# Kernel tuning notes

Measured on AMD Instinct MI355X. Metric: run time of the kernel, lower is better.

## Reference

```python
import jax, jax.numpy as jnp
import numpy as np

B, S, H, K = 64, 512, 768, 21  # batch, seq_len, bert hidden, num_labels


def setup_inputs() -> dict:
    key = jax.random.key(0)
    ks = jax.random.split(key, 8)
    hidden = jax.random.normal(ks[0], (B, S, H), jnp.float32)  # post-BERT states
    W = jax.random.normal(ks[1], (H, K), jnp.float32) * 0.02    # classifier weight
    b = jnp.zeros((K,), jnp.float32)                            # classifier bias
    start_transitions = jax.random.uniform(ks[2], (K,), jnp.float32, -0.1, 0.1)
    transitions = jax.random.uniform(ks[3], (K, K), jnp.float32, -0.1, 0.1)
    end_transitions = jax.random.uniform(ks[4], (K,), jnp.float32, -0.1, 0.1)
    labels = jax.random.randint(ks[5], (B, S), 0, K)
    # torchcrf requires mask[:, 0] == 1; use variable-length prefix masks
    lengths = jax.random.randint(ks[6], (B,), S // 2, S + 1)
    attention_mask = jnp.arange(S)[None, :] < lengths[:, None]  # [B,S] bool
    return dict(hidden=hidden, W=W, b=b,
                start_transitions=start_transitions,
                transitions=transitions,
                end_transitions=end_transitions,
                labels=labels, attention_mask=attention_mask)


def _crf_nll(logits, labels, mask, start_t, trans, end_t):
    """torchcrf CRF forward (reduction='sum' log-likelihood), negated."""
    fmask = mask.astype(logits.dtype)  # [B,S]
    # ---- numerator: score of the gold path ----
    emit = jnp.take_along_axis(logits, labels[..., None], axis=2)[..., 0]  # [B,S]
    tr = trans[labels[:, :-1], labels[:, 1:]]                              # [B,S-1]
    num = start_t[labels[:, 0]] + emit[:, 0] \
        + jnp.sum((emit[:, 1:] + tr) * fmask[:, 1:], axis=1)
    lengths = mask.sum(axis=1)
    last_tags = jnp.take_along_axis(labels, (lengths - 1)[:, None], axis=1)[:, 0]
    num = num + end_t[last_tags]
    # ---- denominator: forward algorithm (logsumexp recurrence) ----
    alpha0 = start_t[None, :] + logits[:, 0]           # [B,K]
    ems = jnp.swapaxes(logits[:, 1:], 0, 1)            # [S-1,B,K]
    ms = jnp.swapaxes(mask[:, 1:], 0, 1)               # [S-1,B]

    def step(alpha, xs):
        em, m = xs
        nxt = jax.scipy.special.logsumexp(
            alpha[:, :, None] + trans[None, :, :] + em[:, None, :], axis=1)
        return jnp.where(m[:, None], nxt, alpha), None

    alpha, _ = jax.lax.scan(step, alpha0, (ems, ms))
    logZ = jax.scipy.special.logsumexp(alpha + end_t[None, :], axis=1)  # [B]
    return jnp.sum(logZ - num)  # negative log-likelihood (sum over batch)


def reference(hidden, W, b, start_transitions, transitions, end_transitions,
              labels, attention_mask):
    # dropout is identity in eval; the GRU in __init__ is unused in forward
    logits = hidden @ W + b  # [B,S,K]
    nll = _crf_nll(logits, labels, attention_mask,
                   start_transitions, transitions, end_transitions)
    # module returns (logits, -1 * log_likelihood) = (logits, nll)
    return (logits, nll)
```

## Files before the change

### kernel.cpp

```cpp
#include <hip/hip_runtime.h>

#define BSZ 64
#define SEQ 512
#define HID 768
#define NK  21
#define NSEG 32
#define SEGLEN 16
#define PSTR 512

typedef short bf16x8 __attribute__((ext_vector_type(8)));
typedef float f32x4  __attribute__((ext_vector_type(4)));

__device__ __forceinline__ unsigned f2bf1(float x) {
    unsigned u = __float_as_uint(x);
    return (u + 0x7fffu + ((u >> 16) & 1u)) >> 16;
}
__device__ __forceinline__ unsigned f2bf_pk(float lo, float hi) {
    return f2bf1(lo) | (f2bf1(hi) << 16);
}

#define U16L(d) __uint_as_float(((unsigned)(d)) << 16)
#define U16H(d) __uint_as_float(((unsigned)(d)) & 0xffff0000u)

__global__ __launch_bounds__(256) void wconv_len_kernel(
    const float* __restrict__ W, const int* __restrict__ mask,
    unsigned short* __restrict__ WT, int* __restrict__ Lbuf,
    float* __restrict__ out)
{
    if (blockIdx.x < 96) {
        const int idx = blockIdx.x * 256 + threadIdx.x;
        const int n = idx / HID;
        const int k = idx - n * HID;
        unsigned short v = 0;
        if (n < NK) v = (unsigned short)f2bf1(W[(size_t)k * NK + n]);
        WT[idx] = v;
    } else {
        const int tid = threadIdx.x;
        if (tid == 255) out[BSZ * SEQ * NK] = 0.f;
        const int b = tid >> 2, q = tid & 3;
        const int* msk = mask + b * SEQ + q * 128;
        int cnt = 0;
        for (int r = 0; r < 128; ++r) cnt += (msk[r] != 0);
        cnt += __shfl_xor(cnt, 1, 64);
        cnt += __shfl_xor(cnt, 2, 64);
        if (q == 0 && b < BSZ) Lbuf[b] = cnt;
    }
}

__global__ __launch_bounds__(256) void gemm_bias_kernel(
    const float* __restrict__ hidden, const unsigned short* __restrict__ WT,
    const float* __restrict__ bias, float* __restrict__ out)
{
    const int tid  = threadIdx.x;
    const int lane = tid & 63;
    const int wv   = tid >> 6;
    const int n    = lane & 15;
    const int quad = lane >> 4;

    const int arow = blockIdx.x * 64 + wv * 16 + n;
    const float* ap = hidden + (size_t)arow * HID + quad * 8;
    const bf16x8* bp0 = (const bf16x8*)(WT + (size_t)n * HID + quad * 8);
    const bf16x8* bp1 = (const bf16x8*)(WT + (size_t)(16 + n) * HID + quad * 8);

    f32x4 acc0 = {0.f, 0.f, 0.f, 0.f};
    f32x4 acc1 = {0.f, 0.f, 0.f, 0.f};

    float4 a0 = *(const float4*)(ap + 0);
    float4 a1 = *(const float4*)(ap + 4);
    float4 p0 = *(const float4*)(ap + 32);
    float4 p1 = *(const float4*)(ap + 36);
    bf16x8 B0 = bp0[0];
    bf16x8 B1 = bp1[0];

    #pragma unroll
    for (int c = 0; c < HID / 32; ++c) {
        float4 q0, q1; bf16x8 Bn0, Bn1;
        if (c + 2 < HID / 32) {
            q0 = *(const float4*)(ap + (c + 2) * 32);
            q1 = *(const float4*)(ap + (c + 2) * 32 + 4);
        }
        if (c + 1 < HID / 32) {
            Bn0 = bp0[(c + 1) * 4];
            Bn1 = bp1[(c + 1) * 4];
        }
        union { bf16x8 v; unsigned u[4]; } af;
        af.u[0] = f2bf_pk(a0.x, a0.y);
        af.u[1] = f2bf_pk(a0.z, a0.w);
        af.u[2] = f2bf_pk(a1.x, a1.y);
        af.u[3] = f2bf_pk(a1.z, a1.w);

        acc0 = __builtin_amdgcn_mfma_f32_16x16x32_bf16(af.v, B0, acc0, 0, 0, 0);
        acc1 = __builtin_amdgcn_mfma_f32_16x16x32_bf16(af.v, B1, acc1, 0, 0, 0);

        a0 = p0; a1 = p1; p0 = q0; p1 = q1;
        B0 = Bn0; B1 = Bn1;
    }

    const float b0v = bias[n];
    const float b1v = (n < NK - 16) ? bias[16 + n] : 0.f;
    const int rbase = blockIdx.x * 64 + wv * 16 + quad * 4;
    #pragma unroll
    for (int r = 0; r < 4; ++r) {
        float* op = out + (size_t)(rbase + r) * NK;
        op[n] = acc0[r] + b0v;
        if (n < NK - 16) op[16 + n] = acc1[r] + b1v;
    }
}

#define EHI(u) __uint_as_float((u) & 0xffff0000u)
#define ELO(u) __uint_as_float((u) << 16)
__global__ __launch_bounds__(64, 2) void prepass_kernel(
    const float* __restrict__ logits, const float* __restrict__ trans,
    const int* __restrict__ Lbuf,
    unsigned short* __restrict__ Nrowb, unsigned short* __restrict__ Ncolb,
    float* __restrict__ rlog)
{
    const int bs   = blockIdx.x;
    const int b    = bs >> 5;
    const int s    = bs & 31;
    const int lane = threadIdx.x;
    int g = lane / 21; if (g > 2) g = 2;
    int i = lane - g * 21; if (i > 20) i = 20;
    const int j0 = 7 * g;

    const int L = Lbuf[b];

    unsigned Epk[7][11];
    #pragma unroll
    for (int jl = 0; jl < 7; ++jl)
        #pragma unroll
        for (int p = 0; p < 11; ++p) {
            const float ehi = __expf(trans[(2 * p) * NK + j0 + jl]);
            const float elo = (2 * p + 1 < 21)
                            ? __expf(trans[(2 * p + 1) * NK + j0 + jl]) : 0.f;
            Epk[jl][p] = (f2bf1(ehi) << 16) | f2bf1(elo);
        }

    const float* lg = logits + (size_t)b * SEQ * NK;

    float P[7];
    float rl = 0.f;
    const int t0 = s * SEGLEN + 1;

    if (t0 < L) {
        const float C = lg[t0 * NK];
        rl = C;
        #pragma unroll
        for (int jl = 0; jl < 7; ++jl)
            P[jl] = __expf(trans[i * NK + j0 + jl])
                  * __expf(lg[t0 * NK + j0 + jl] - C);
    } else {
        #pragma unroll
        for (int jl = 0; jl < 7; ++jl) P[jl] = (i == j0 + jl) ? 1.f : 0.f;
    }

#define BPF(v, idx) __uint_as_float(__builtin_amdgcn_ds_bpermute((idx) * 4, __float_as_uint(v)))

    #pragma unroll
    for (int u = 1; u < SEGLEN; ++u) {
        const int t = t0 + u;
        if (t < L) {
            float row[22];
            #pragma unroll
            for (int k = 0; k < 21; ++k)
                row[k] = BPF(P[k % 7], (k / 7) * 21 + i);
            row[21] = 0.f;

            const float C = lg[t * NK];
            rl += C;
            float X[7];
            #pragma unroll
            for (int jl = 0; jl < 7; ++jl)
                X[jl] = __expf(lg[t * NK + j0 + jl] - C);

            #pragma unroll
            for (int jl = 0; jl < 7; ++jl) {
                float s0 = 0.f, s1 = 0.f;
                #pragma unroll
                for (int p = 0; p < 11; ++p) {
                    const unsigned e = Epk[jl][p];
                    s0 = fmaf(row[2 * p    ], EHI(e), s0);
                    s1 = fmaf(row[2 * p + 1], ELO(e), s1);
                }
                P[jl] = (s0 + s1) * X[jl];
            }
            const float m = BPF(P[0], 0);
            const float r = __builtin_amdgcn_rcpf(m);
            #pragma unroll
            for (int jl = 0; jl < 7; ++jl) P[jl] *= r;
            rl += __logf(m);
        }
    }
#undef BPF

    if (lane < 63) {
        unsigned short* nr = Nrowb + (size_t)bs * PSTR + i * 24 + j0;
        #pragma unroll
        for (int jl = 0; jl < 7; ++jl) nr[jl] = (unsigned short)f2bf1(P[jl]);
        unsigned short* nc = Ncolb + (size_t)bs * PSTR + i;
        #pragma unroll
        for (int jl = 0; jl < 7; ++jl)
            nc[(j0 + jl) * 24] = (unsigned short)f2bf1(P[jl]);
    }
    if (lane == 0) rlog[bs] = rl;
}

__global__ __launch_bounds__(128) void scan_kernel(
    const float* __restrict__ logits,
    const float* __restrict__ start_t,
    const float* __restrict__ trans,
    const float* __restrict__ end_t,
    const int* __restrict__ labels,
    const int* __restrict__ Lbuf,
    const unsigned short* __restrict__ Nrowb,
    const unsigned short* __restrict__ Ncolb,
    const float* __restrict__ rlog,
    float* __restrict__ out)
{
    __shared__ float comb[26];

    const int b    = blockIdx.x;
    const int tid  = threadIdx.x;
    const int lane = tid & 63;
    const int wid  = tid >> 6;

    const float* lg = logits + (size_t)b * SEQ * NK;
    const int* lab = labels + b * SEQ;
    const int L = Lbuf[b];

    {
        float numacc = 0.f;
        for (int t = tid; t < L; t += 128) {
            if (t == 0) numacc += start_t[lab[0]] + lg[lab[0]];
            else        numacc += lg[t * NK + lab[t]] + trans[lab[t - 1] * NK + lab[t]];
        }
        if (tid == 0) numacc += end_t[lab[L - 1]];
        #pragma unroll
        for (int off = 32; off > 0; off >>= 1) numacc += __shfl_xor(numacc, off, 64);
        if (lane == 0) comb[22 + wid] = numacc;
    }

    float rls = (lane < 16) ? rlog[b * NSEG + wid * 16 + lane] : 0.f;
    #pragma unroll
    for (int off = 32; off > 0; off >>= 1) rls += __shfl_xor(rls, off, 64);

    const int jj = (lane < NK) ? lane : NK - 1;

#define RL(v, k) __uint_as_float(__builtin_amdgcn_readlane(__float_as_uint(v), k))
#define PMV(vv, c0, c1, c2, outv) do {                                        \
    float s0 = RL(vv, 0) * U16L(c0.x);                                        \
    float s1 = RL(vv, 1) * U16H(c0.x);                                        \
    float s2 = RL(vv, 2) * U16L(c0.y);                                        \
    s0 = fmaf(RL(vv,  3), U16H(c0.y), s0); s1 = fmaf(RL(vv,  4), U16L(c0.z), s1); \
    s2 = fmaf(RL(vv,  5), U16H(c0.z), s2); s0 = fmaf(RL(vv,  6), U16L(c0.w), s0); \
    s1 = fmaf(RL(vv,  7), U16H(c0.w), s1); s2 = fmaf(RL(vv,  8), U16L(c1.x), s2); \
    s0 = fmaf(RL(vv,  9), U16H(c1.x), s0); s1 = fmaf(RL(vv, 10), U16L(c1.y), s1); \
    s2 = fmaf(RL(vv, 11), U16H(c1.y), s2); s0 = fmaf(RL(vv, 12), U16L(c1.z), s0); \
    s1 = fmaf(RL(vv, 13), U16H(c1.z), s1); s2 = fmaf(RL(vv, 14), U16L(c1.w), s2); \
    s0 = fmaf(RL(vv, 15), U16H(c1.w), s0); s1 = fmaf(RL(vv, 16), U16L(c2.x), s1); \
    s2 = fmaf(RL(vv, 17), U16H(c2.x), s2); s0 = fmaf(RL(vv, 18), U16L(c2.y), s0); \
    s1 = fmaf(RL(vv, 19), U16H(c2.y), s1); s2 = fmaf(RL(vv, 20), U16L(c2.z), s2); \
    outv = (s0 + s1) + s2;                                                    \
} while (0)

    float a, Orenorm = 0.f;
    int4 c0, c1, c2, n0, n1, n2;

    if (wid == 0) {
        a = __expf(start_t[jj]) * __expf(lg[jj] - lg[0]);

        const char* base = (const char*)(Ncolb + (size_t)b * NSEG * PSTR) + jj * 48;
        c0 = *(const int4*)(base);
        c1 = *(const int4*)(base + 16);
        c2 = *(const int4*)(base + 32);
        for (int s = 0; s < 16; ++s) {
            if (s < 15) {
                const char* p = base + (size_t)(s + 1) * (PSTR * 2);
                n0 = *(const int4*)(p);
                n1 = *(const int4*)(p + 16);
                n2 = *(const int4*)(p + 32);
            }
            float nv; PMV(a, c0, c1, c2, nv); a = nv;
            const float m = __uint_as_float(
                __builtin_amdgcn_readfirstlane(__float_as_uint(a)));
            a *= __builtin_amdgcn_rcpf(m);
            Orenorm += __logf(m);
            c0 = n0; c1 = n1; c2 = n2;
        }
    } else {
        a = __expf(end_t[jj]);

        const char* base = (const char*)(Nrowb + (size_t)b * NSEG * PSTR) + jj * 48;
        {
            const char* p = base + (size_t)31 * (PSTR * 2);
            c0 = *(const int4*)(p);
            c1 = *(const int4*)(p + 16);
            c2 = *(const int4*)(p + 32);
        }
        for (int s = 31; s >= 16; --s) {
            if (s > 16) {
                const char* p = base + (size_t)(s - 1) * (PSTR * 2);
                n0 = *(const int4*)(p);
                n1 = *(const int4*)(p + 16);
                n2 = *(const int4*)(p + 32);
            }
            float nv; PMV(a, c0, c1, c2, nv); a = nv;
            const float m = __uint_as_float(
                __builtin_amdgcn_readfirstlane(__float_as_uint(a)));
            a *= __builtin_amdgcn_rcpf(m);
            Orenorm += __logf(m);
            c0 = n0; c1 = n1; c2 = n2;
        }
    }
#undef RL
#undef PMV

    if (wid == 1) {
        if (lane < NK) comb[lane] = a;
        if (lane == 0) comb[21] = Orenorm + rls;
    }
    __syncthreads();

    if (wid == 0) {
        float val = (lane < NK) ? a * comb[lane] : 0.f;
        #pragma unroll
        for (int off = 32; off > 0; off >>= 1) val += __shfl_xor(val, off, 64);
        if (lane == 0) {
            const float OF  = Orenorm + rls + lg[0];
            const float num = comb[22] + comb[23];
            atomicAdd(out + BSZ * SEQ * NK, OF + comb[21] + __logf(val) - num);
        }
    }
}

extern "C" void kernel_launch(void* const* d_in, const int* in_sizes, int n_in,
                              void* d_out, int out_size, void* d_ws, size_t ws_size,
                              hipStream_t stream)
{
    const float* hidden  = (const float*)d_in[0];
    const float* W       = (const float*)d_in[1];
    const float* bias    = (const float*)d_in[2];
    const float* start_t = (const float*)d_in[3];
    const float* trans   = (const float*)d_in[4];
    const float* end_t   = (const float*)d_in[5];
    const int*   labels  = (const int*)d_in[6];
    const int*   mask    = (const int*)d_in[7];
    float* out = (float*)d_out;

    char* ws = (char*)d_ws;
    unsigned short* WT    = (unsigned short*)ws;
    int*            Lbuf  = (int*)(ws + 65536);
    float*          rlog  = (float*)(ws + 69632);
    unsigned short* Nrowb = (unsigned short*)(ws + 131072);
    unsigned short* Ncolb = (unsigned short*)(ws + 131072 + 2 * 1024 * 1024);

    wconv_len_kernel<<<97, 256, 0, stream>>>(W, mask, WT, Lbuf, out);
    gemm_bias_kernel<<<(BSZ * SEQ) / 64, 256, 0, stream>>>(hidden, WT, bias, out);
    prepass_kernel<<<BSZ * NSEG, 64, 0, stream>>>(out, trans, Lbuf, Nrowb, Ncolb, rlog);
    scan_kernel<<<BSZ, 128, 0, stream>>>(out, start_t, trans, end_t, labels, Lbuf,
                                         Nrowb, Ncolb, rlog, out);
}
```

Measured before the change: 204.4 us.

## Split GEMM K dimension across two waves with LDS reduction

Each GEMM block now covers 16 rows instead of 64, and its two waves each handle half of the 768-wide hidden dimension. The partial accumulators are combined through shared memory before bias is added and the result stored. This gives four times as many blocks and halves the serial chain of MFMA steps per wave, which should raise occupancy and memory-level parallelism on the bandwidth-bound 100MB read. In exchange it adds a barrier, LDS traffic and more block launches, and each block re-reads W for fewer rows.

```diff
diff --git a/kernel.cpp b/kernel.cpp
--- a/kernel.cpp
+++ b/kernel.cpp
@@ -47,20 +47,23 @@
     }
 }
 
-__global__ __launch_bounds__(256) void gemm_bias_kernel(
+__global__ __launch_bounds__(128) void gemm_bias_kernel(
     const float* __restrict__ hidden, const unsigned short* __restrict__ WT,
     const float* __restrict__ bias, float* __restrict__ out)
 {
+    __shared__ float part0[16][16];
+    __shared__ float part1[16][16];
+
     const int tid  = threadIdx.x;
     const int lane = tid & 63;
     const int wv   = tid >> 6;
     const int n    = lane & 15;
     const int quad = lane >> 4;
 
-    const int arow = blockIdx.x * 64 + wv * 16 + n;
-    const float* ap = hidden + (size_t)arow * HID + quad * 8;
-    const bf16x8* bp0 = (const bf16x8*)(WT + (size_t)n * HID + quad * 8);
-    const bf16x8* bp1 = (const bf16x8*)(WT + (size_t)(16 + n) * HID + quad * 8);
+    const int arow = blockIdx.x * 16 + n;
+    const float* ap = hidden + (size_t)arow * HID + wv * 384 + quad * 8;
+    const bf16x8* bp0 = (const bf16x8*)(WT + (size_t)n * HID + wv * 384 + quad * 8);
+    const bf16x8* bp1 = (const bf16x8*)(WT + (size_t)(16 + n) * HID + wv * 384 + quad * 8);
 
     f32x4 acc0 = {0.f, 0.f, 0.f, 0.f};
     f32x4 acc1 = {0.f, 0.f, 0.f, 0.f};
@@ -73,13 +76,13 @@
     bf16x8 B1 = bp1[0];
 
     #pragma unroll
-    for (int c = 0; c < HID / 32; ++c) {
+    for (int c = 0; c < 12; ++c) {
         float4 q0, q1; bf16x8 Bn0, Bn1;
-        if (c + 2 < HID / 32) {
+        if (c + 2 < 12) {
             q0 = *(const float4*)(ap + (c + 2) * 32);
             q1 = *(const float4*)(ap + (c + 2) * 32 + 4);
         }
-        if (c + 1 < HID / 32) {
+        if (c + 1 < 12) {
             Bn0 = bp0[(c + 1) * 4];
             Bn1 = bp1[(c + 1) * 4];
         }
@@ -96,14 +99,26 @@
         B0 = Bn0; B1 = Bn1;
     }
 
-    const float b0v = bias[n];
-    const float b1v = (n < NK - 16) ? bias[16 + n] : 0.f;
-    const int rbase = blockIdx.x * 64 + wv * 16 + quad * 4;
-    #pragma unroll
-    for (int r = 0; r < 4; ++r) {
-        float* op = out + (size_t)(rbase + r) * NK;
-        op[n] = acc0[r] + b0v;
-        if (n < NK - 16) op[16 + n] = acc1[r] + b1v;
+    if (wv == 1) {
+        #pragma unroll
+        for (int r = 0; r < 4; ++r) {
+            part0[quad * 4 + r][n] = acc0[r];
+            part1[quad * 4 + r][n] = acc1[r];
+        }
+    }
+    __syncthreads();
+
+    if (wv == 0) {
+        const float b0v = bias[n];
+        const float b1v = (n < NK - 16) ? bias[16 + n] : 0.f;
+        const int rbase = blockIdx.x * 16 + quad * 4;
+        #pragma unroll
+        for (int r = 0; r < 4; ++r) {
+            float* op = out + (size_t)(rbase + r) * NK;
+            op[n] = acc0[r] + part0[quad * 4 + r][n] + b0v;
+            if (n < NK - 16)
+                op[16 + n] = acc1[r] + part1[quad * 4 + r][n] + b1v;
+        }
     }
 }
 
@@ -355,7 +370,7 @@
     unsigned short* Ncolb = (unsigned short*)(ws + 131072 + 2 * 1024 * 1024);
 
     wconv_len_kernel<<<97, 256, 0, stream>>>(W, mask, WT, Lbuf, out);
-    gemm_bias_kernel<<<(BSZ * SEQ) / 64, 256, 0, stream>>>(hidden, WT, bias, out);
+    gemm_bias_kernel<<<(BSZ * SEQ) / 16, 128, 0, stream>>>(hidden, WT, bias, out);
     prepass_kernel<<<BSZ * NSEG, 64, 0, stream>>>(out, trans, Lbuf, Nrowb, Ncolb, rlog);
     scan_kernel<<<BSZ, 128, 0, stream>>>(out, start_t, trans, end_t, labels, Lbuf,
                                          Nrowb, Ncolb, rlog, out);
```

Result: no change. 204.6 us (+0.1%).
